# Kernel optimization log

Hardware: AMD Instinct MI355X
Metric: run time of the kernel (lower is better)

The kernel has to match this reference:

```python
import jax, jax.numpy as jnp
import numpy as np
import math

B, S, D, H = 4, 2048, 1024, 16
DK = D // H

def setup_inputs() -> dict:
    key = jax.random.key(0)
    ks = jax.random.split(key, 11)
    mk = lambda k, shape: jax.random.normal(k, shape, dtype=jnp.float32)
    inp = {
        'query': mk(ks[0], (B, S, D)),
        'key':   mk(ks[1], (B, S, D)),
        'value': mk(ks[2], (B, S, D)),
        'Wq': mk(ks[3], (D, D)) * 0.02, 'bq': jnp.zeros((D,), jnp.float32),
        'Wk': mk(ks[4], (D, D)) * 0.02, 'bk': jnp.zeros((D,), jnp.float32),
        'Wv': mk(ks[5], (D, D)) * 0.02, 'bv': jnp.zeros((D,), jnp.float32),
        'Wo': mk(ks[6], (D, D)) * 0.02, 'bo': jnp.zeros((D,), jnp.float32),
    }
    return inp

def reference(query, key, value, Wq, bq, Wk, bk, Wv, bv, Wo, bo):
    b, s, d = query.shape
    scale = 1.0 / math.sqrt(DK)
    def proj(x, W, bias):
        # nn.Linear: x @ W.T + b, then split heads -> [b, h, s, dk]
        return (x @ W.T + bias).reshape(b, s, H, DK).transpose(0, 2, 1, 3)
    q = proj(query, Wq, bq)
    k = proj(key, Wk, bk)
    v = proj(value, Wv, bv)
    scores = jnp.einsum('bhqd,bhkd->bhqk', q, k) * scale  # [b,h,s,s]
    attn = jax.nn.softmax(scores, axis=-1)
    # dropout is identity in eval/reference mode
    x = jnp.einsum('bhqk,bhkd->bhqd', attn, v)
    x = x.transpose(0, 2, 1, 3).reshape(b, s, d)
    return x @ Wo.T + bo
```

## Files before the change

### kernel.cpp

```cpp
#include <hip/hip_runtime.h>
#include <stdint.h>

#define DEV static __device__ __forceinline__

typedef __bf16 bf16_t;
typedef bf16_t bf16x8 __attribute__((ext_vector_type(8)));
typedef bf16_t bf16x4 __attribute__((ext_vector_type(4)));
typedef float f32x4 __attribute__((ext_vector_type(4)));

static constexpr int Bc = 4, Sc = 2048, Dc = 1024, Hc = 16, DKc = 64;
static constexpr int Mrows = Bc * Sc;

DEV unsigned short f2bf(float f) {
  unsigned int u = __float_as_uint(f);
  u += 0x7fffu + ((u >> 16) & 1u);
  return (unsigned short)(u >> 16);
}

DEV float fexp2(float x) {
#if __has_builtin(__builtin_amdgcn_exp2f)
  return __builtin_amdgcn_exp2f(x);
#else
  return exp2f(x);
#endif
}

#if __has_builtin(__builtin_amdgcn_mfma_f32_16x16x16_bf16)
DEV f32x4 mfma16(bf16x4 a, bf16x4 b, f32x4 c) {
  return __builtin_amdgcn_mfma_f32_16x16x16_bf16(a, b, c, 0, 0, 0);
}
#elif __has_builtin(__builtin_amdgcn_mfma_f32_16x16x16bf16_1k)
typedef short s16x4 __attribute__((ext_vector_type(4)));
DEV f32x4 mfma16(bf16x4 a, bf16x4 b, f32x4 c) {
  union U { bf16x4 h; s16x4 s; };
  U ua, ub; ua.h = a; ub.h = b;
  return __builtin_amdgcn_mfma_f32_16x16x16bf16_1k(ua.s, ub.s, c, 0, 0, 0);
}
#else
DEV f32x4 mfma16(bf16x4 a, bf16x4 b, f32x4 c) {
  asm("v_mfma_f32_16x16x16_bf16 %0, %1, %2, %0" : "+v"(c) : "v"(a), "v"(b));
  return c;
}
#endif

DEV void gload_lds16(const void* g, void* l) {
  __builtin_amdgcn_global_load_lds(
      (const __attribute__((address_space(1))) void*)g,
      (__attribute__((address_space(3))) void*)l, 16, 0, 0);
}

__global__ void __launch_bounds__(256) cvt_bf16_seg_kernel(
    const float* __restrict__ s0, const float* __restrict__ s1,
    const float* __restrict__ s2, const float* __restrict__ s3,
    unsigned short* __restrict__ out, int lg) {
  int i = blockIdx.x * blockDim.x + threadIdx.x;
  int seg = i >> lg, j = i & ((1 << lg) - 1);
  const float* src = seg == 0 ? s0 : seg == 1 ? s1 : seg == 2 ? s2 : s3;
  float4 v = reinterpret_cast<const float4*>(src)[j];
  ushort4 o;
  o.x = f2bf(v.x); o.y = f2bf(v.y); o.z = f2bf(v.z); o.w = f2bf(v.w);
  reinterpret_cast<ushort4*>(out)[i] = o;
}

template <bool QKV>
__global__ void __launch_bounds__(256) gemm_dbuf_kernel(
    const unsigned short* __restrict__ A0, const unsigned short* __restrict__ A1,
    const unsigned short* __restrict__ A2,
    const unsigned short* __restrict__ W0, const unsigned short* __restrict__ W1,
    const unsigned short* __restrict__ W2,
    const float* __restrict__ b0, const float* __restrict__ b1,
    const float* __restrict__ b2,
    void* __restrict__ C0, void* __restrict__ C1, void* __restrict__ C2,
    int M, int N, int K, float scale0) {
  __shared__ unsigned short lA[3][128 * 32];
  __shared__ unsigned short lB[3][128 * 32];
  const int t = threadIdx.x;
  const int wv = t >> 6, ln = t & 63;
  const int l15 = ln & 15, lhi = ln >> 4;

  const unsigned short* A; const unsigned short* W;
  const float* bias; void* Cout; float scale; int mode;
  if (QKV) {
    const int z = blockIdx.z;
    A = z == 0 ? A0 : z == 1 ? A1 : A2;
    W = z == 0 ? W0 : z == 1 ? W1 : W2;
    bias = z == 0 ? b0 : z == 1 ? b1 : b2;
    Cout = z == 0 ? C0 : z == 1 ? C1 : C2;
    scale = z == 0 ? scale0 : 1.0f;
    mode = z == 2 ? 2 : 1;
  } else {
    A = A0; W = W0; bias = b0; Cout = C0; scale = scale0; mode = 0;
  }

  const int nwg = gridDim.x * gridDim.y;
  const int hw = blockIdx.y * gridDim.x + blockIdx.x;
  const int chunk = nwg >> 3;
  const int swzid = (hw & 7) * chunk + (hw >> 3);
  const int m0 = (swzid / gridDim.x) * 128, n0 = (swzid % gridDim.x) * 128;
  const int wr = wv >> 1, wc = wv & 1;
  const int swzR = (l15 & 3) << 4;

  const int rowA = t >> 2;
  const int colS = ((t & 3) ^ (rowA & 3)) * 8;
  const unsigned short* aS = A + (size_t)(m0 + rowA) * K + colS;
  const unsigned short* wS = W + (size_t)(n0 + rowA) * K + colS;
  const size_t rstep = (size_t)64 * K;
  const int d0 = t * 16, d1 = 4096 + t * 16;

  f32x4 acc[4][4] = {};

#define GSTAGE(bi, k0_)                                        \
  do {                                                         \
    gload_lds16(aS + (k0_), (char*)lA[bi] + d0);               \
    gload_lds16(aS + rstep + (k0_), (char*)lA[bi] + d1);       \
    gload_lds16(wS + (k0_), (char*)lB[bi] + d0);               \
    gload_lds16(wS + rstep + (k0_), (char*)lB[bi] + d1);       \
  } while (0)

  GSTAGE(0, 0);
  GSTAGE(1, 32);

  const int NK = K >> 5;
  int cur = 0, stg = 2;
  for (int tk = 0; tk < NK; ++tk) {
    if (tk == NK - 1)
      asm volatile("s_waitcnt vmcnt(0)" ::: "memory");
    else
      asm volatile("s_waitcnt vmcnt(4)" ::: "memory");
    __builtin_amdgcn_s_barrier();
    __builtin_amdgcn_sched_barrier(0);

    if (tk + 2 < NK) GSTAGE(stg, (tk + 2) * 32);

    bf16x8 af[4], bfr[4];
#pragma unroll
    for (int i = 0; i < 4; ++i)
      af[i] = *reinterpret_cast<const bf16x8*>(
          (char*)lA[cur] + (((wr * 64 + i * 16 + l15) * 64 + lhi * 16) ^ swzR));
#pragma unroll
    for (int j = 0; j < 4; ++j)
      bfr[j] = *reinterpret_cast<const bf16x8*>(
          (char*)lB[cur] + (((wc * 64 + j * 16 + l15) * 64 + lhi * 16) ^ swzR));
#pragma unroll
    for (int i = 0; i < 4; ++i)
#pragma unroll
      for (int j = 0; j < 4; ++j)
        acc[i][j] = __builtin_amdgcn_mfma_f32_16x16x32_bf16(af[i], bfr[j], acc[i][j], 0, 0, 0);

    cur = cur == 2 ? 0 : cur + 1;
    stg = stg == 2 ? 0 : stg + 1;
  }
#undef GSTAGE

#pragma unroll
  for (int i = 0; i < 4; ++i)
#pragma unroll
    for (int j = 0; j < 4; ++j) {
      int n = n0 + wc * 64 + j * 16 + l15;
      float bv = bias[n];
      if (QKV && mode == 2) {
        int mb = m0 + wr * 64 + i * 16 + lhi * 4;
        int sl = mb & (Sc - 1);
        int pl = (sl & ~60) | ((sl & 48) >> 2) | ((sl & 12) << 2);
        ushort4 ov;
        ov.x = f2bf((acc[i][j][0] + bv) * scale);
        ov.y = f2bf((acc[i][j][1] + bv) * scale);
        ov.z = f2bf((acc[i][j][2] + bv) * scale);
        ov.w = f2bf((acc[i][j][3] + bv) * scale);
        *reinterpret_cast<ushort4*>((unsigned short*)Cout +
            ((size_t)(mb >> 11) * Dc + n) * Sc + pl) = ov;
      } else {
#pragma unroll
        for (int jj = 0; jj < 4; ++jj) {
          int m = m0 + wr * 64 + i * 16 + lhi * 4 + jj;
          float v = (acc[i][j][jj] + bv) * scale;
          if (QKV)
            ((unsigned short*)Cout)[(size_t)m * N + n] = f2bf(v);
          else
            ((float*)Cout)[(size_t)m * N + n] = v;
        }
      }
    }
}

__global__ void __launch_bounds__(512, 4) attn_kernel(
    const unsigned short* __restrict__ Q, const unsigned short* __restrict__ Kk,
    const unsigned short* __restrict__ Vt, unsigned short* __restrict__ X) {
  __shared__ unsigned short lK[2][128 * 64];
  __shared__ unsigned short lVT[2][64 * 128];
  const int t = threadIdx.x;
  const int wv = t >> 6, ln = t & 63;
  const int l15 = ln & 15, lhi = ln >> 4;
  const int q0 = blockIdx.x * 128;
  const int h = blockIdx.y, b = blockIdx.z;
  const size_t base = (size_t)b * Sc * Dc;
  const int hoff = h * DKc;

  bf16x8 qf[2];
  {
    const unsigned short* qp = Q + base + (size_t)(q0 + wv * 16 + l15) * Dc + hoff + lhi * 8;
    qf[0] = *reinterpret_cast<const bf16x8*>(qp);
    qf[1] = *reinterpret_cast<const bf16x8*>(qp + 32);
  }

  const int kvr = t >> 3;
  const int kcol = ((t & 7) * 8) ^ ((kvr & 7) << 3);
  const unsigned short* kS = Kk + base + (size_t)kvr * Dc + hoff + kcol;
  const int vdk = t >> 4;
  const int vkv = ((t & 15) * 8) ^ ((vdk & 7) << 3);
  const unsigned short* vS = Vt + ((size_t)b * Dc + hoff + vdk) * Sc + vkv;

  float nm = 0.f;
  f32x4 xacc[4] = {};
  f32x4 lsum = {};
  const int swzK = (l15 & 7) << 4;

  bf16x4 ones4;
#pragma unroll
  for (int i = 0; i < 4; ++i) ones4[i] = (bf16_t)1.0f;

#define DSTAGE(bi, kv0_)                                                        \
  do {                                                                          \
    gload_lds16(kS + (size_t)(kv0_)*Dc, (char*)lK[bi] + t * 16);                \
    gload_lds16(kS + (size_t)((kv0_) + 64) * Dc, (char*)lK[bi] + 8192 + t * 16);\
    gload_lds16(vS + (kv0_), (char*)lVT[bi] + t * 16);                          \
    gload_lds16(vS + (size_t)32 * Sc + (kv0_), (char*)lVT[bi] + 8192 + t * 16); \
  } while (0)

  DSTAGE(0, 0);
  asm volatile("s_waitcnt vmcnt(0)" ::: "memory");
  __builtin_amdgcn_s_barrier();
  __builtin_amdgcn_sched_barrier(0);

  const int NT2 = Sc / 128;
  for (int tt = 0; tt < NT2; ++tt) {
    const int cur = tt & 1;
    if (tt + 1 < NT2) DSTAGE(cur ^ 1, (tt + 1) * 128);

    const char* K_ = (const char*)lK[cur];
    const char* VT_ = (const char*)lVT[cur];

    f32x4 nm4 = {nm, nm, nm, nm};
    f32x4 sacc[2][4];
    __builtin_amdgcn_s_setprio(1);
#pragma unroll
    for (int s64 = 0; s64 < 2; ++s64)
#pragma unroll
      for (int ct = 0; ct < 4; ++ct) {
        f32x4 z = nm4;
#pragma unroll
        for (int kk = 0; kk < 2; ++kk) {
          bf16x8 kf = *reinterpret_cast<const bf16x8*>(
              K_ + (((s64 * 64 + ct * 16 + l15) * 128 + kk * 64 + lhi * 16) ^ swzK));
          z = __builtin_amdgcn_mfma_f32_16x16x32_bf16(kf, qf[kk], z, 0, 0, 0);
        }
        sacc[s64][ct] = z;
      }
    __builtin_amdgcn_s_setprio(0);

    float m0a = fmaxf(fmaxf(sacc[0][0][0], sacc[0][0][1]), fmaxf(sacc[0][0][2], sacc[0][0][3]));
    float m0b = fmaxf(fmaxf(sacc[0][1][0], sacc[0][1][1]), fmaxf(sacc[0][1][2], sacc[0][1][3]));
    float m0c = fmaxf(fmaxf(sacc[0][2][0], sacc[0][2][1]), fmaxf(sacc[0][2][2], sacc[0][2][3]));
    float m0d = fmaxf(fmaxf(sacc[0][3][0], sacc[0][3][1]), fmaxf(sacc[0][3][2], sacc[0][3][3]));
    float m1a = fmaxf(fmaxf(sacc[1][0][0], sacc[1][0][1]), fmaxf(sacc[1][0][2], sacc[1][0][3]));
    float m1b = fmaxf(fmaxf(sacc[1][1][0], sacc[1][1][1]), fmaxf(sacc[1][1][2], sacc[1][1][3]));
    float m1c = fmaxf(fmaxf(sacc[1][2][0], sacc[1][2][1]), fmaxf(sacc[1][2][2], sacc[1][2][3]));
    float m1d = fmaxf(fmaxf(sacc[1][3][0], sacc[1][3][1]), fmaxf(sacc[1][3][2], sacc[1][3][3]));
    float mt = fmaxf(fmaxf(fmaxf(m0a, m0b), fmaxf(m0c, m0d)),
                     fmaxf(fmaxf(m1a, m1b), fmaxf(m1c, m1d)));

    if (__any(mt > 8.0f)) {
      float mtr = fmaxf(mt, __shfl_xor(mt, 16));
      mtr = fmaxf(mtr, __shfl_xor(mtr, 32));
      float mte = fmaxf(mtr, 0.f);
      float corr = fexp2(-mte);
      nm -= mte;
#pragma unroll
      for (int jj = 0; jj < 4; ++jj) {
        float cO = __shfl(corr, lhi * 4 + jj);
        lsum[jj] *= cO;
#pragma unroll
        for (int dt = 0; dt < 4; ++dt) xacc[dt][jj] *= cO;
      }
#pragma unroll
      for (int s64 = 0; s64 < 2; ++s64)
#pragma unroll
        for (int ct = 0; ct < 4; ++ct)
#pragma unroll
          for (int jj = 0; jj < 4; ++jj) sacc[s64][ct][jj] -= mte;
    }

    __builtin_amdgcn_s_setprio(1);
#pragma unroll
    for (int s64 = 0; s64 < 2; ++s64) {
      bf16x4 pa[4];
#pragma unroll
      for (int ct = 0; ct < 4; ++ct)
#pragma unroll
        for (int jj = 0; jj < 4; ++jj)
          pa[ct][jj] = (bf16_t)fexp2(sacc[s64][ct][jj]);
#pragma unroll
      for (int ct = 0; ct < 4; ++ct) lsum = mfma16(pa[ct], ones4, lsum);
#pragma unroll
      for (int dt = 0; dt < 4; ++dt) {
#pragma unroll
        for (int sel = 0; sel < 2; ++sel) {
          bf16x8 vb2 = *reinterpret_cast<const bf16x8*>(
              VT_ + (((dt * 16 + l15) * 256 + s64 * 128 + lhi * 32 + sel * 16) ^ swzK));
          bf16x4 vlo = __builtin_shufflevector(vb2, vb2, 0, 1, 2, 3);
          bf16x4 vhi = __builtin_shufflevector(vb2, vb2, 4, 5, 6, 7);
          xacc[dt] = mfma16(pa[2 * sel + 0], vlo, xacc[dt]);
          xacc[dt] = mfma16(pa[2 * sel + 1], vhi, xacc[dt]);
        }
      }
    }
    __builtin_amdgcn_s_setprio(0);

    asm volatile("s_waitcnt vmcnt(0)" ::: "memory");
    __builtin_amdgcn_s_barrier();
    __builtin_amdgcn_sched_barrier(0);
  }
#undef DSTAGE

  float iO[4];
#pragma unroll
  for (int jj = 0; jj < 4; ++jj) iO[jj] = 1.0f / lsum[jj];

  unsigned short* xp = X + base + (size_t)(q0 + wv * 16) * Dc + hoff;
#pragma unroll
  for (int dt = 0; dt < 4; ++dt)
#pragma unroll
    for (int jj = 0; jj < 4; ++jj) {
      int r = lhi * 4 + jj;
      xp[(size_t)r * Dc + dt * 16 + l15] = f2bf(xacc[dt][jj] * iO[jj]);
    }
}

extern "C" void kernel_launch(void* const* d_in, const int* in_sizes, int n_in,
                              void* d_out, int out_size, void* d_ws, size_t ws_size,
                              hipStream_t stream) {
  const float* query = (const float*)d_in[0];
  const float* key   = (const float*)d_in[1];
  const float* value = (const float*)d_in[2];
  const float* Wq = (const float*)d_in[3];
  const float* bq = (const float*)d_in[4];
  const float* Wk = (const float*)d_in[5];
  const float* bk = (const float*)d_in[6];
  const float* Wv = (const float*)d_in[7];
  const float* bv = (const float*)d_in[8];
  const float* Wo = (const float*)d_in[9];
  const float* bo = (const float*)d_in[10];

  const size_t NBS = (size_t)Mrows * Dc;
  const size_t NW  = (size_t)Dc * Dc;
  unsigned short* bQin = (unsigned short*)d_ws;
  unsigned short* bKin = bQin + NBS;
  unsigned short* bVin = bKin + NBS;
  unsigned short* bWq  = bVin + NBS;
  unsigned short* bWk  = bWq + NW;
  unsigned short* bWv  = bWk + NW;
  unsigned short* bWo  = bWv + NW;
  unsigned short* Qp   = bWo + NW;
  unsigned short* Kp   = Qp + NBS;
  unsigned short* Vtp  = Kp + NBS;
  unsigned short* Xp   = Vtp + NBS;

  cvt_bf16_seg_kernel<<<(int)(3 * NBS / 1024), 256, 0, stream>>>(
      query, key, value, value, bQin, 21);
  cvt_bf16_seg_kernel<<<(int)(4 * NW / 1024), 256, 0, stream>>>(
      Wq, Wk, Wv, Wo, bWq, 18);

  gemm_dbuf_kernel<true><<<dim3(Dc / 128, Mrows / 128, 3), 256, 0, stream>>>(
      bQin, bKin, bVin, bWq, bWk, bWv, bq, bk, bv, Qp, Kp, Vtp,
      Mrows, Dc, Dc, 0.125f * 1.44269504088896340736f);

  attn_kernel<<<dim3(Sc / 128, Hc, Bc), 512, 0, stream>>>(Qp, Kp, Vtp, Xp);

  gemm_dbuf_kernel<false><<<dim3(Dc / 128, Mrows / 128, 1), 256, 0, stream>>>(
      Xp, nullptr, nullptr, bWo, nullptr, nullptr, bo, nullptr, nullptr,
      d_out, nullptr, nullptr, Mrows, Dc, Dc, 1.0f);
}
```

Baseline: 228.8 us.

## Fuse fp32-to-bf16 input conversion into QKV GEMM A-tile loads

Removes the separate conversion kernel for query/key/value and has the QKV GEMM load fp32 activations, convert them in registers and store bf16 into LDS. This avoids writing and re-reading a bf16 copy of the activations. The GEMM pipeline changes from triple-buffered async LDS loads to a double-buffered scheme with a full wait each iteration. That reduces load/compute overlap and also affects the output projection GEMM.

```diff
diff --git a/kernel.cpp b/kernel.cpp
--- a/kernel.cpp
+++ b/kernel.cpp
@@ -47,6 +47,13 @@
   __builtin_amdgcn_global_load_lds(
       (const __attribute__((address_space(1))) void*)g,
       (__attribute__((address_space(3))) void*)l, 16, 0, 0);
+}
+
+DEV bf16x8 cvt8(float4 a, float4 b) {
+  bf16x8 r;
+  r[0] = (bf16_t)a.x; r[1] = (bf16_t)a.y; r[2] = (bf16_t)a.z; r[3] = (bf16_t)a.w;
+  r[4] = (bf16_t)b.x; r[5] = (bf16_t)b.y; r[6] = (bf16_t)b.z; r[7] = (bf16_t)b.w;
+  return r;
 }
 
 __global__ void __launch_bounds__(256) cvt_bf16_seg_kernel(
@@ -64,32 +71,32 @@
 
 template <bool QKV>
 __global__ void __launch_bounds__(256) gemm_dbuf_kernel(
-    const unsigned short* __restrict__ A0, const unsigned short* __restrict__ A1,
-    const unsigned short* __restrict__ A2,
+    const void* __restrict__ A0v, const void* __restrict__ A1v,
+    const void* __restrict__ A2v,
     const unsigned short* __restrict__ W0, const unsigned short* __restrict__ W1,
     const unsigned short* __restrict__ W2,
     const float* __restrict__ b0, const float* __restrict__ b1,
     const float* __restrict__ b2,
     void* __restrict__ C0, void* __restrict__ C1, void* __restrict__ C2,
     int M, int N, int K, float scale0) {
-  __shared__ unsigned short lA[3][128 * 32];
-  __shared__ unsigned short lB[3][128 * 32];
+  __shared__ unsigned short lA[2][128 * 32];
+  __shared__ unsigned short lB[2][128 * 32];
   const int t = threadIdx.x;
   const int wv = t >> 6, ln = t & 63;
   const int l15 = ln & 15, lhi = ln >> 4;
 
-  const unsigned short* A; const unsigned short* W;
+  const void* Av; const unsigned short* W;
   const float* bias; void* Cout; float scale; int mode;
   if (QKV) {
     const int z = blockIdx.z;
-    A = z == 0 ? A0 : z == 1 ? A1 : A2;
+    Av = z == 0 ? A0v : z == 1 ? A1v : A2v;
     W = z == 0 ? W0 : z == 1 ? W1 : W2;
     bias = z == 0 ? b0 : z == 1 ? b1 : b2;
     Cout = z == 0 ? C0 : z == 1 ? C1 : C2;
     scale = z == 0 ? scale0 : 1.0f;
     mode = z == 2 ? 2 : 1;
   } else {
-    A = A0; W = W0; bias = b0; Cout = C0; scale = scale0; mode = 0;
+    Av = A0v; W = W0; bias = b0; Cout = C0; scale = scale0; mode = 0;
   }
 
   const int nwg = gridDim.x * gridDim.y;
@@ -102,35 +109,58 @@
 
   const int rowA = t >> 2;
   const int colS = ((t & 3) ^ (rowA & 3)) * 8;
-  const unsigned short* aS = A + (size_t)(m0 + rowA) * K + colS;
   const unsigned short* wS = W + (size_t)(n0 + rowA) * K + colS;
   const size_t rstep = (size_t)64 * K;
   const int d0 = t * 16, d1 = 4096 + t * 16;
+  const float* aF = QKV ? (const float*)Av + (size_t)(m0 + rowA) * K + colS : nullptr;
+  const unsigned short* aB =
+      QKV ? nullptr : (const unsigned short*)Av + (size_t)(m0 + rowA) * K + colS;
 
   f32x4 acc[4][4] = {};
 
-#define GSTAGE(bi, k0_)                                        \
+#define WSTAGE(bi, k0_)                                        \
   do {                                                         \
-    gload_lds16(aS + (k0_), (char*)lA[bi] + d0);               \
-    gload_lds16(aS + rstep + (k0_), (char*)lA[bi] + d1);       \
     gload_lds16(wS + (k0_), (char*)lB[bi] + d0);               \
     gload_lds16(wS + rstep + (k0_), (char*)lB[bi] + d1);       \
   } while (0)
-
-  GSTAGE(0, 0);
-  GSTAGE(1, 32);
+#define ABSTAGE(bi, k0_)                                       \
+  do {                                                         \
+    gload_lds16(aB + (k0_), (char*)lA[bi] + d0);               \
+    gload_lds16(aB + rstep + (k0_), (char*)lA[bi] + d1);       \
+  } while (0)
+
+  WSTAGE(0, 0);
+  if (QKV) {
+    float4 a0 = *(const float4*)(aF);
+    float4 a1 = *(const float4*)(aF + 4);
+    float4 a2 = *(const float4*)(aF + rstep);
+    float4 a3 = *(const float4*)(aF + rstep + 4);
+    *reinterpret_cast<bf16x8*>((char*)lA[0] + d0) = cvt8(a0, a1);
+    *reinterpret_cast<bf16x8*>((char*)lA[0] + d1) = cvt8(a2, a3);
+  } else {
+    ABSTAGE(0, 0);
+  }
+  asm volatile("s_waitcnt vmcnt(0) lgkmcnt(0)" ::: "memory");
+  __builtin_amdgcn_s_barrier();
+  __builtin_amdgcn_sched_barrier(0);
 
   const int NK = K >> 5;
-  int cur = 0, stg = 2;
   for (int tk = 0; tk < NK; ++tk) {
-    if (tk == NK - 1)
-      asm volatile("s_waitcnt vmcnt(0)" ::: "memory");
-    else
-      asm volatile("s_waitcnt vmcnt(4)" ::: "memory");
-    __builtin_amdgcn_s_barrier();
-    __builtin_amdgcn_sched_barrier(0);
-
-    if (tk + 2 < NK) GSTAGE(stg, (tk + 2) * 32);
+    const int cur = tk & 1, nxt = cur ^ 1;
+    float4 a0, a1, a2, a3;
+    const bool pre = (tk + 1 < NK);
+    if (pre) {
+      WSTAGE(nxt, (tk + 1) * 32);
+      if (QKV) {
+        const float* p = aF + (tk + 1) * 32;
+        a0 = *(const float4*)(p);
+        a1 = *(const float4*)(p + 4);
+        a2 = *(const float4*)(p + rstep);
+        a3 = *(const float4*)(p + rstep + 4);
+      } else {
+        ABSTAGE(nxt, (tk + 1) * 32);
+      }
+    }
 
     bf16x8 af[4], bfr[4];
 #pragma unroll
@@ -147,10 +177,17 @@
       for (int j = 0; j < 4; ++j)
         acc[i][j] = __builtin_amdgcn_mfma_f32_16x16x32_bf16(af[i], bfr[j], acc[i][j], 0, 0, 0);
 
-    cur = cur == 2 ? 0 : cur + 1;
-    stg = stg == 2 ? 0 : stg + 1;
+    if (QKV && pre) {
+      *reinterpret_cast<bf16x8*>((char*)lA[nxt] + d0) = cvt8(a0, a1);
+      *reinterpret_cast<bf16x8*>((char*)lA[nxt] + d1) = cvt8(a2, a3);
+    }
+
+    asm volatile("s_waitcnt vmcnt(0) lgkmcnt(0)" ::: "memory");
+    __builtin_amdgcn_s_barrier();
+    __builtin_amdgcn_sched_barrier(0);
   }
-#undef GSTAGE
+#undef WSTAGE
+#undef ABSTAGE
 
 #pragma unroll
   for (int i = 0; i < 4; ++i)
@@ -353,10 +390,7 @@
 
   const size_t NBS = (size_t)Mrows * Dc;
   const size_t NW  = (size_t)Dc * Dc;
-  unsigned short* bQin = (unsigned short*)d_ws;
-  unsigned short* bKin = bQin + NBS;
-  unsigned short* bVin = bKin + NBS;
-  unsigned short* bWq  = bVin + NBS;
+  unsigned short* bWq  = (unsigned short*)d_ws;
   unsigned short* bWk  = bWq + NW;
   unsigned short* bWv  = bWk + NW;
   unsigned short* bWo  = bWv + NW;
@@ -365,13 +399,11 @@
   unsigned short* Vtp  = Kp + NBS;
   unsigned short* Xp   = Vtp + NBS;
 
-  cvt_bf16_seg_kernel<<<(int)(3 * NBS / 1024), 256, 0, stream>>>(
-      query, key, value, value, bQin, 21);
   cvt_bf16_seg_kernel<<<(int)(4 * NW / 1024), 256, 0, stream>>>(
       Wq, Wk, Wv, Wo, bWq, 18);
 
   gemm_dbuf_kernel<true><<<dim3(Dc / 128, Mrows / 128, 3), 256, 0, stream>>>(
-      bQin, bKin, bVin, bWq, bWk, bWv, bq, bk, bv, Qp, Kp, Vtp,
+      query, key, value, bWq, bWk, bWv, bq, bk, bv, Qp, Kp, Vtp,
       Mrows, Dc, Dc, 0.125f * 1.44269504088896340736f);
 
   attn_kernel<<<dim3(Sc / 128, Hc, Bc), 512, 0, stream>>>(Qp, Kp, Vtp, Xp);
```

Result: no change. 226.1 us (-1.2%).
